# Optimization experiments

Hardware: AMD Instinct MI355X
Metric: run time of the kernel (lower is better)

## Reference

```python
import jax, jax.numpy as jnp
import numpy as np

N, E, IN_FEATS, HID, HEADS = 50000, 800000, 256, 32, 8
NEG_SLOPE = 0.2


def _init_params(key):
    ks = jax.random.split(key, 12)
    def lin(k, fi, fo):
        return jax.random.normal(k, (fi, fo), jnp.float32) * (1.0 / np.sqrt(fi))
    p = {}
    # layer 0: in_feats -> HID x HEADS
    p['W0'] = lin(ks[0], IN_FEATS, HEADS * HID)
    p['al0'] = jax.random.normal(ks[1], (HEADS, HID), jnp.float32) * 0.1
    p['ar0'] = jax.random.normal(ks[2], (HEADS, HID), jnp.float32) * 0.1
    p['b0'] = jnp.zeros((HEADS * HID,), jnp.float32)
    # layer 1: HID*HEADS -> HID x HEADS
    p['W1'] = lin(ks[3], HEADS * HID, HEADS * HID)
    p['al1'] = jax.random.normal(ks[4], (HEADS, HID), jnp.float32) * 0.1
    p['ar1'] = jax.random.normal(ks[5], (HEADS, HID), jnp.float32) * 0.1
    p['b1'] = jnp.zeros((HEADS * HID,), jnp.float32)
    # layer 2 (final): HID*HEADS -> HID x 1 head, no activation
    p['W2'] = lin(ks[6], HEADS * HID, HID)
    p['al2'] = jax.random.normal(ks[7], (1, HID), jnp.float32) * 0.1
    p['ar2'] = jax.random.normal(ks[8], (1, HID), jnp.float32) * 0.1
    p['b2'] = jnp.zeros((HID,), jnp.float32)
    return p


def setup_inputs() -> dict:
    key = jax.random.key(0)
    k1, k2, k3, kp = jax.random.split(key, 4)
    inp = {
        'features': jax.random.normal(k1, (N, IN_FEATS), jnp.float32),
        'src': jax.random.randint(k2, (E,), 0, N, jnp.int32),
        'dst': jax.random.randint(k3, (E,), 0, N, jnp.int32),
    }
    inp.update(_init_params(kp))
    return inp


def _gat_layer(x, src, dst, W, al, ar, b, heads, act):
    n = x.shape[0]
    d = W.shape[1] // heads
    feat = (x @ W).reshape(n, heads, d)           # [N,H,D]
    el = jnp.sum(feat * al, axis=-1)              # [N,H]
    er = jnp.sum(feat * ar, axis=-1)              # [N,H]
    e = jax.nn.leaky_relu(el[src] + er[dst], NEG_SLOPE)   # [E,H]
    # segment softmax over destination neighborhoods
    emax = jax.ops.segment_max(e, dst, num_segments=n)
    ex = jnp.exp(e - emax[dst])
    denom = jax.ops.segment_sum(ex, dst, num_segments=n)
    a = ex / (denom[dst] + 1e-9)                  # [E,H]
    msg = feat[src] * a[:, :, None]               # [E,H,D]
    out = jax.ops.segment_sum(msg, dst, num_segments=n)   # [N,H,D]
    out = out + b.reshape(1, heads, d)
    return act(out) if act is not None else out


def reference(features, src, dst, W0, al0, ar0, b0, W1, al1, ar1, b1, W2, al2, ar2, b2):
    h = _gat_layer(features, src, dst, W0, al0, ar0, b0, HEADS, jax.nn.elu)
    h = h.reshape(h.shape[0], -1)
    h = _gat_layer(h, src, dst, W1, al1, ar1, b1, HEADS, jax.nn.elu)
    h = h.reshape(h.shape[0], -1)
    h = _gat_layer(h, src, dst, W2, al2, ar2, b2, 1, None)   # [N,1,D]
    return h.mean(axis=1)                                    # [N,D]
```

## Files before the change

### kernel.cpp

```cpp
#include <hip/hip_runtime.h>

typedef unsigned short u16;
typedef unsigned int   u32;
typedef __attribute__((ext_vector_type(8))) short  short8;
typedef __attribute__((ext_vector_type(4))) float  f32x4;
typedef __attribute__((ext_vector_type(2))) float  f32x2;
typedef __attribute__((ext_vector_type(2))) unsigned int u32v2;
typedef __attribute__((ext_vector_type(4))) unsigned int u32v4;

#define NN 50000
#define NE 800000

__device__ __forceinline__ float bf2f(u16 b) { return __uint_as_float(((u32)b) << 16); }
__device__ __forceinline__ float bflo(u32 p) { return __uint_as_float(p << 16); }
__device__ __forceinline__ float bfhi(u32 p) { return __uint_as_float(p & 0xffff0000u); }
__device__ __forceinline__ u16 f2bf(float f) {
    u32 u = __float_as_uint(f);
    u32 r = u + 0x7fffu + ((u >> 16) & 1u);
    return (u16)(r >> 16);
}
__device__ __forceinline__ float lexp(float v) {
    v = v > 0.f ? v : 0.2f * v;
    return __expf(fminf(v, 60.f));
}

struct DetectArgs { const u32* p[13]; int nw[13]; };

__global__ __launch_bounds__(256) void k_detect(DetectArgs a, int* flags) {
    __shared__ int sh[256], sz[256];
    int j = blockIdx.x;
    const u32* x = a.p[j];
    int n = a.nw[j];
    int t = threadIdx.x;
    int hits = 0, nz = 0;
    for (int i = t; i < n; i += 256) {
        u32 w = x[i];
        if (w) {
            ++nz;
            u32 e = (w >> 7) & 0xffu;
            if (e >= 100 && e <= 150) ++hits;
        }
    }
    sh[t] = hits; sz[t] = nz;
    __syncthreads();
    for (int ofs = 128; ofs > 0; ofs >>= 1) {
        if (t < ofs) { sh[t] += sh[t + ofs]; sz[t] += sz[t + ofs]; }
        __syncthreads();
    }
    if (t == 0) flags[j] = (sz[0] == 0) ? 2 : ((sh[0] * 2 >= sz[0]) ? 0 : 1);
}

struct ConvArgs { const void* s[9]; float* d[9]; int n[9]; int fi[9]; };

__global__ void k_convert(ConvArgs a, const int* __restrict__ flags) {
    int j = blockIdx.y;
    int i = blockIdx.x * 256 + threadIdx.x;
    if (i >= a.n[j]) return;
    int fl = flags[a.fi[j]];
    float v = 0.f;
    if (fl == 1) v = ((const float*)a.s[j])[i];
    else if (fl == 0) v = bf2f(((const u16*)a.s[j])[i]);
    a.d[j][i] = v;
}

__global__ void k_wpack(const void* __restrict__ Wsrc, const int* __restrict__ flags,
                        int fidx, int N, u16* __restrict__ Wp, int nchunks) {
    int id = blockIdx.x * 256 + threadIdx.x;
    if (id >= nchunks) return;
    int L = id & 63, kt = (id >> 6) & 7, nt = id >> 9;
    int col = nt * 16 + (L & 15);
    int krow = kt * 32 + ((L >> 4) & 3) * 8;
    bool isf32 = (flags[fidx] == 1);
#pragma unroll
    for (int j = 0; j < 8; ++j) {
        int s = (krow + j) * N + col;
        Wp[id * 8 + j] = isf32 ? f2bf(((const float*)Wsrc)[s]) : ((const u16*)Wsrc)[s];
    }
}

__global__ void k_hist(const int* __restrict__ dst, int* __restrict__ deg, int E) {
    int e = blockIdx.x * 256 + threadIdx.x;
    if (e < E) atomicAdd(&deg[dst[e]], 1);
}

__global__ __launch_bounds__(256) void k_scan_partial(const int* __restrict__ deg,
                                                      int* __restrict__ bsum, int n) {
    __shared__ int red[256];
    int t = threadIdx.x;
    int i = blockIdx.x * 256 + t;
    red[t] = (i < n) ? deg[i] : 0;
    __syncthreads();
    for (int ofs = 128; ofs > 0; ofs >>= 1) {
        if (t < ofs) red[t] += red[t + ofs];
        __syncthreads();
    }
    if (t == 0) bsum[blockIdx.x] = red[0];
}

__global__ __launch_bounds__(256) void k_scan_bsum(int* __restrict__ bsum, int nb) {
    __shared__ int s[256];
    int t = threadIdx.x;
    int v = (t < nb) ? bsum[t] : 0;
    s[t] = v;
    __syncthreads();
    for (int ofs = 1; ofs < 256; ofs <<= 1) {
        int x = (t >= ofs) ? s[t - ofs] : 0;
        __syncthreads();
        s[t] += x;
        __syncthreads();
    }
    if (t < nb) bsum[t] = s[t] - v;
}

__global__ __launch_bounds__(256) void k_scan_final(const int* __restrict__ deg,
                                                    const int* __restrict__ bsum,
                                                    int* __restrict__ rowptr,
                                                    int* __restrict__ cursor, int n) {
    __shared__ int s[256];
    int t = threadIdx.x;
    int i = blockIdx.x * 256 + t;
    int v = (i < n) ? deg[i] : 0;
    s[t] = v;
    __syncthreads();
    for (int ofs = 1; ofs < 256; ofs <<= 1) {
        int x = (t >= ofs) ? s[t - ofs] : 0;
        __syncthreads();
        s[t] += x;
        __syncthreads();
    }
    int excl = bsum[blockIdx.x] + s[t] - v;
    if (i < n) {
        rowptr[i] = excl;
        cursor[i] = excl;
        if (i == n - 1) rowptr[n] = excl + v;
    }
}

__global__ void k_scatter(const int* __restrict__ src, const int* __restrict__ dst,
                          int* __restrict__ cursor, int* __restrict__ csr_src, int E) {
    int e = blockIdx.x * 256 + threadIdx.x;
    if (e >= E) return;
    int p = atomicAdd(&cursor[dst[e]], 1);
    csr_src[p] = src[e];
}

__global__ __launch_bounds__(256) void k_gemm_mfma(const void* __restrict__ Xv,
                                                   const int* __restrict__ xflag,
                                                   const u16* __restrict__ Wp,
                                                   u16* __restrict__ OUT, int nrows) {
    __shared__ u16 As[64 * 256];
    const int t = threadIdx.x;
    const int w = t >> 6, L = t & 63;
    const int quad = (L >> 4) & 3;
    const int r0 = blockIdx.x * 64;
    const int nb = blockIdx.y * 8;
    const bool xf32 = (xflag != nullptr) && (*xflag == 1);

    short8* Asv = (short8*)As;
    short8 zero = {0, 0, 0, 0, 0, 0, 0, 0};
#pragma unroll
    for (int i = 0; i < 8; ++i) {
        int g = i * 256 + t;
        int row = g >> 5, cc = g & 31;
        int r = r0 + row;
        short8 val = zero;
        if (r < nrows) {
            if (xf32) {
                const f32x4* Xf4 = (const f32x4*)Xv;
                f32x4 lo = Xf4[(size_t)r * 64 + cc * 2];
                f32x4 hi = Xf4[(size_t)r * 64 + cc * 2 + 1];
                val[0] = (short)f2bf(lo[0]); val[1] = (short)f2bf(lo[1]);
                val[2] = (short)f2bf(lo[2]); val[3] = (short)f2bf(lo[3]);
                val[4] = (short)f2bf(hi[0]); val[5] = (short)f2bf(hi[1]);
                val[6] = (short)f2bf(hi[2]); val[7] = (short)f2bf(hi[3]);
            } else {
                val = ((const short8*)Xv)[(size_t)r * 32 + cc];
            }
        }
        Asv[cc * 64 + row] = val;
    }

    const short8* Wv = (const short8*)Wp;
    short8 bf[2][8];
#pragma unroll
    for (int jn = 0; jn < 2; ++jn) {
        int nt = nb + w + jn * 4;
#pragma unroll
        for (int kt = 0; kt < 8; ++kt) bf[jn][kt] = Wv[(nt * 8 + kt) * 64 + L];
    }
    __syncthreads();

    f32x4 acc[4][2];
#pragma unroll
    for (int mi = 0; mi < 4; ++mi)
#pragma unroll
        for (int jn = 0; jn < 2; ++jn) acc[mi][jn] = (f32x4){0.f, 0.f, 0.f, 0.f};

#pragma unroll
    for (int kt = 0; kt < 8; ++kt) {
#pragma unroll
        for (int mi = 0; mi < 4; ++mi) {
            short8 af = Asv[(kt * 4 + quad) * 64 + mi * 16 + (L & 15)];
            acc[mi][0] = __builtin_amdgcn_mfma_f32_16x16x32_bf16(af, bf[0][kt], acc[mi][0], 0, 0, 0);
            acc[mi][1] = __builtin_amdgcn_mfma_f32_16x16x32_bf16(af, bf[1][kt], acc[mi][1], 0, 0, 0);
        }
    }

    const int colbase = blockIdx.y * 128;
#pragma unroll
    for (int mi = 0; mi < 4; ++mi) {
        int rb = r0 + mi * 16 + quad * 4;
#pragma unroll
        for (int jn = 0; jn < 2; ++jn) {
            int c = colbase + (w + jn * 4) * 16 + (L & 15);
#pragma unroll
            for (int reg = 0; reg < 4; ++reg) {
                int r = rb + reg;
                if (r < nrows) OUT[(size_t)r * 256 + c] = f2bf(acc[mi][jn][reg]);
            }
        }
    }
}

__global__ __launch_bounds__(256) void k_gemm_mfma32(const u16* __restrict__ Xb,
                                                     const u16* __restrict__ Wp,
                                                     u16* __restrict__ OUT, int nrows) {
    __shared__ u16 As[128 * 256];
    const int t = threadIdx.x;
    const int w = t >> 6, L = t & 63;
    const int quad = (L >> 4) & 3;
    const int r0 = blockIdx.x * 128;
    const int mh = (w >> 1) * 64, nt = w & 1;

    const short8* Xv = (const short8*)Xb;
    short8* Asv = (short8*)As;
    short8 zero = {0, 0, 0, 0, 0, 0, 0, 0};
#pragma unroll
    for (int i = 0; i < 16; ++i) {
        int g = i * 256 + t;
        int row = g >> 5, cc = g & 31;
        int r = r0 + row;
        Asv[cc * 128 + row] = (r < nrows) ? Xv[(size_t)r * 32 + cc] : zero;
    }

    const short8* Wv = (const short8*)Wp;
    short8 bf[8];
#pragma unroll
    for (int kt = 0; kt < 8; ++kt) bf[kt] = Wv[(nt * 8 + kt) * 64 + L];
    __syncthreads();

    f32x4 acc[4];
#pragma unroll
    for (int mi = 0; mi < 4; ++mi) acc[mi] = (f32x4){0.f, 0.f, 0.f, 0.f};

#pragma unroll
    for (int kt = 0; kt < 8; ++kt) {
#pragma unroll
        for (int mi = 0; mi < 4; ++mi) {
            short8 af = Asv[(kt * 4 + quad) * 128 + mh + mi * 16 + (L & 15)];
            acc[mi] = __builtin_amdgcn_mfma_f32_16x16x32_bf16(af, bf[kt], acc[mi], 0, 0, 0);
        }
    }

#pragma unroll
    for (int mi = 0; mi < 4; ++mi) {
        int rb = r0 + mh + mi * 16 + quad * 4;
        int c = nt * 16 + (L & 15);
#pragma unroll
        for (int reg = 0; reg < 4; ++reg) {
            int r = rb + reg;
            if (r < nrows) OUT[(size_t)r * 32 + c] = f2bf(acc[mi][reg]);
        }
    }
}

__global__ void k_elr8(const u16* __restrict__ featb, const float* __restrict__ al,
                       const float* __restrict__ ar, float* __restrict__ el,
                       float* __restrict__ er, int n) {
    int idx = blockIdx.x * 256 + threadIdx.x;
    if (idx >= n * 8) return;
    int node = idx >> 3, h = idx & 7;
    const u32v4* fu = (const u32v4*)((const u32*)featb + (size_t)node * 128 + h * 16);
    const float* A = al + h * 32;
    const float* B = ar + h * 32;
    float sl = 0.f, sr = 0.f;
#pragma unroll
    for (int j = 0; j < 4; ++j) {
        u32v4 w4 = fu[j];
#pragma unroll
        for (int k = 0; k < 4; ++k) {
            u32 w = (k == 0) ? w4.x : (k == 1) ? w4.y : (k == 2) ? w4.z : w4.w;
            float f0 = bflo(w), f1 = bfhi(w);
            int c = j * 8 + k * 2;
            sl += f0 * A[c] + f1 * A[c + 1];
            sr += f0 * B[c] + f1 * B[c + 1];
        }
    }
    el[idx] = sl;
    er[idx] = sr;
}

__global__ void k_elr1(const u16* __restrict__ featb, const float* __restrict__ al,
                       const float* __restrict__ ar, float* __restrict__ el,
                       float* __restrict__ er, int n) {
    int node = blockIdx.x * 256 + threadIdx.x;
    if (node >= n) return;
    const u32v4* fu = (const u32v4*)((const u32*)featb + (size_t)node * 16);
    float sl = 0.f, sr = 0.f;
#pragma unroll
    for (int j = 0; j < 4; ++j) {
        u32v4 w4 = fu[j];
#pragma unroll
        for (int k = 0; k < 4; ++k) {
            u32 w = (k == 0) ? w4.x : (k == 1) ? w4.y : (k == 2) ? w4.z : w4.w;
            float f0 = bflo(w), f1 = bfhi(w);
            int c = j * 8 + k * 2;
            sl += f0 * al[c] + f1 * al[c + 1];
            sr += f0 * ar[c] + f1 * ar[c + 1];
        }
    }
    el[node] = sl;
    er[node] = sr;
}

__global__ __launch_bounds__(256) void k_gather8(const int* __restrict__ rowptr,
                                                 const int* __restrict__ csr_src,
                                                 const float* __restrict__ el,
                                                 const float* __restrict__ er,
                                                 const u32v2* __restrict__ featb4,
                                                 const float* __restrict__ bias,
                                                 u32v2* __restrict__ xout4) {
    int t = threadIdx.x;
    int d = blockIdx.x * 4 + (t >> 6);
    int q = t & 63;
    int h = q >> 3;
    int b = rowptr[d], e = rowptr[d + 1];
    float erd = er[d * 8 + h];
    float a0 = 0.f, a1 = 0.f, a2 = 0.f, a3 = 0.f, ssum = 0.f;
    int p = b;
    for (; p + 4 <= e; p += 4) {
        int s0 = csr_src[p], s1 = csr_src[p + 1], s2 = csr_src[p + 2], s3 = csr_src[p + 3];
        float e0 = lexp(el[s0 * 8 + h] + erd);
        float e1 = lexp(el[s1 * 8 + h] + erd);
        float e2 = lexp(el[s2 * 8 + h] + erd);
        float e3 = lexp(el[s3 * 8 + h] + erd);
        u32v2 w0 = featb4[(size_t)s0 * 64 + q];
        u32v2 w1 = featb4[(size_t)s1 * 64 + q];
        u32v2 w2 = featb4[(size_t)s2 * 64 + q];
        u32v2 w3 = featb4[(size_t)s3 * 64 + q];
        a0 += bflo(w0.x) * e0; a1 += bfhi(w0.x) * e0; a2 += bflo(w0.y) * e0; a3 += bfhi(w0.y) * e0;
        a0 += bflo(w1.x) * e1; a1 += bfhi(w1.x) * e1; a2 += bflo(w1.y) * e1; a3 += bfhi(w1.y) * e1;
        a0 += bflo(w2.x) * e2; a1 += bfhi(w2.x) * e2; a2 += bflo(w2.y) * e2; a3 += bfhi(w2.y) * e2;
        a0 += bflo(w3.x) * e3; a1 += bfhi(w3.x) * e3; a2 += bflo(w3.y) * e3; a3 += bfhi(w3.y) * e3;
        ssum += (e0 + e1) + (e2 + e3);
    }
    for (; p < e; ++p) {
        int s = csr_src[p];
        float ev = lexp(el[s * 8 + h] + erd);
        u32v2 w = featb4[(size_t)s * 64 + q];
        a0 += bflo(w.x) * ev; a1 += bfhi(w.x) * ev;
        a2 += bflo(w.y) * ev; a3 += bfhi(w.y) * ev;
        ssum += ev;
    }
    float rd = 1.f / (ssum + 1e-9f);
    const float4 bb = *(const float4*)&bias[4 * q];
    float v0 = a0 * rd + bb.x;
    float v1 = a1 * rd + bb.y;
    float v2 = a2 * rd + bb.z;
    float v3 = a3 * rd + bb.w;
    v0 = v0 > 0.f ? v0 : expm1f(v0);
    v1 = v1 > 0.f ? v1 : expm1f(v1);
    v2 = v2 > 0.f ? v2 : expm1f(v2);
    v3 = v3 > 0.f ? v3 : expm1f(v3);
    u32v2 o;
    o.x = (u32)f2bf(v0) | ((u32)f2bf(v1) << 16);
    o.y = (u32)f2bf(v2) | ((u32)f2bf(v3) << 16);
    xout4[(size_t)d * 64 + q] = o;
}

__global__ __launch_bounds__(256) void k_gather1(const int* __restrict__ rowptr,
                                                 const int* __restrict__ csr_src,
                                                 const float* __restrict__ el,
                                                 const float* __restrict__ er,
                                                 const u32* __restrict__ featb2,
                                                 const float* __restrict__ bias,
                                                 void* __restrict__ out,
                                                 const int* __restrict__ flag, int n) {
    int t = threadIdx.x;
    int d = blockIdx.x * 16 + (t >> 4);
    int q = t & 15;
    if (d >= n) return;
    int b = rowptr[d], e = rowptr[d + 1];
    float erd = er[d];
    float a0 = 0.f, a1 = 0.f, ssum = 0.f;
    int p = b;
    for (; p + 4 <= e; p += 4) {
        int s0 = csr_src[p], s1 = csr_src[p + 1], s2 = csr_src[p + 2], s3 = csr_src[p + 3];
        float e0 = lexp(el[s0] + erd);
        float e1 = lexp(el[s1] + erd);
        float e2 = lexp(el[s2] + erd);
        float e3 = lexp(el[s3] + erd);
        u32 w0 = featb2[(size_t)s0 * 16 + q];
        u32 w1 = featb2[(size_t)s1 * 16 + q];
        u32 w2 = featb2[(size_t)s2 * 16 + q];
        u32 w3 = featb2[(size_t)s3 * 16 + q];
        a0 += bflo(w0) * e0; a1 += bfhi(w0) * e0;
        a0 += bflo(w1) * e1; a1 += bfhi(w1) * e1;
        a0 += bflo(w2) * e2; a1 += bfhi(w2) * e2;
        a0 += bflo(w3) * e3; a1 += bfhi(w3) * e3;
        ssum += (e0 + e1) + (e2 + e3);
    }
    for (; p < e; ++p) {
        int s = csr_src[p];
        float ev = lexp(el[s] + erd);
        u32 w = featb2[(size_t)s * 16 + q];
        a0 += bflo(w) * ev;
        a1 += bfhi(w) * ev;
        ssum += ev;
    }
    float rd = 1.f / (ssum + 1e-9f);
    float v0 = a0 * rd + bias[2 * q];
    float v1 = a1 * rd + bias[2 * q + 1];
    if (*flag == 1) {
        f32x2 o = {v0, v1};
        ((f32x2*)out)[(size_t)d * 16 + q] = o;
    } else {
        ((u32*)out)[(size_t)d * 16 + q] = (u32)f2bf(v0) | ((u32)f2bf(v1) << 16);
    }
}

extern "C" void kernel_launch(void* const* d_in, const int* in_sizes, int n_in,
                              void* d_out, int out_size, void* d_ws, size_t ws_size,
                              hipStream_t stream) {
    const void* features = d_in[0];
    const int* src = (const int*)d_in[1];
    const int* dst = (const int*)d_in[2];

    char* ws = (char*)d_ws;
    size_t off = 0;
    auto carve = [&](size_t bytes) -> void* {
        void* p = ws + off;
        off = (off + bytes + 255) & ~(size_t)255;
        return p;
    };
    int*   flags = (int*)carve(64);
    float* pconv = (float*)carve(2048 * 4);
    u16*   Wp0 = (u16*)carve(65536 * 2);
    u16*   Wp1 = (u16*)carve(65536 * 2);
    u16*   Wp2 = (u16*)carve(8192 * 2);
    u16*   Xb    = (u16*)carve((size_t)NN * 256 * 2);
    u16*   featb = (u16*)carve((size_t)NN * 256 * 2);
    float* el   = (float*)carve((size_t)NN * 8 * 4);
    float* er   = (float*)carve((size_t)NN * 8 * 4);
    int*   deg     = (int*)carve((size_t)NN * 4);
    int*   cursor  = (int*)carve((size_t)NN * 4);
    int*   rowptr  = (int*)carve((size_t)(NN + 1) * 4);
    int*   bsum    = (int*)carve(256 * 4);
    int*   csr_src = (int*)carve((size_t)NE * 4);
    if (off > ws_size) return;

    const int N = NN, E = NE;
    const int nscan = (N + 255) / 256;

    DetectArgs da;
    const int din_idx[13] = {0, 3, 4, 5, 6, 7, 8, 9, 10, 11, 12, 13, 14};
    for (int j = 0; j < 13; ++j) {
        da.p[j] = (const u32*)d_in[din_idx[j]];
        int nw = in_sizes[din_idx[j]] / 2;
        da.nw[j] = nw > 512 ? 512 : nw;
    }
    k_detect<<<13, 256, 0, stream>>>(da, flags);

    ConvArgs ca;
    const int psl[9] = {4, 5, 6, 8, 9, 10, 12, 13, 14};
    const int pfl[9] = {2, 3, 4, 6, 7, 8, 10, 11, 12};
    float* dsts[9];
    {
        size_t o = 0;
        for (int j = 0; j < 9; ++j) {
            dsts[j] = pconv + o;
            o += (size_t)in_sizes[psl[j]];
        }
    }
    for (int j = 0; j < 9; ++j) {
        ca.s[j] = d_in[psl[j]];
        ca.d[j] = dsts[j];
        ca.n[j] = in_sizes[psl[j]];
        ca.fi[j] = pfl[j];
    }
    k_convert<<<dim3(1, 9), 256, 0, stream>>>(ca, flags);
    float* al0f = dsts[0]; float* ar0f = dsts[1]; float* b0f = dsts[2];
    float* al1f = dsts[3]; float* ar1f = dsts[4]; float* b1f = dsts[5];
    float* al2f = dsts[6]; float* ar2f = dsts[7]; float* b2f = dsts[8];

    k_wpack<<<32, 256, 0, stream>>>(d_in[3],  flags, 1, 256, Wp0, 8192);
    k_wpack<<<32, 256, 0, stream>>>(d_in[7],  flags, 5, 256, Wp1, 8192);
    k_wpack<<<4,  256, 0, stream>>>(d_in[11], flags, 9, 32,  Wp2, 1024);

    hipMemsetAsync(deg, 0, (size_t)N * 4, stream);
    k_hist<<<(E + 255) / 256, 256, 0, stream>>>(dst, deg, E);
    k_scan_partial<<<nscan, 256, 0, stream>>>(deg, bsum, N);
    k_scan_bsum<<<1, 256, 0, stream>>>(bsum, nscan);
    k_scan_final<<<nscan, 256, 0, stream>>>(deg, bsum, rowptr, cursor, N);
    k_scatter<<<(E + 255) / 256, 256, 0, stream>>>(src, dst, cursor, csr_src, E);

    const dim3 ggrid((N + 63) / 64, 2);

    k_gemm_mfma<<<ggrid, 256, 0, stream>>>(features, flags, Wp0, featb, N);
    k_elr8<<<(N * 8 + 255) / 256, 256, 0, stream>>>(featb, al0f, ar0f, el, er, N);
    k_gather8<<<N / 4, 256, 0, stream>>>(rowptr, csr_src, el, er,
                                         (const u32v2*)featb, b0f, (u32v2*)Xb);

    k_gemm_mfma<<<ggrid, 256, 0, stream>>>(Xb, nullptr, Wp1, featb, N);
    k_elr8<<<(N * 8 + 255) / 256, 256, 0, stream>>>(featb, al1f, ar1f, el, er, N);
    k_gather8<<<N / 4, 256, 0, stream>>>(rowptr, csr_src, el, er,
                                         (const u32v2*)featb, b1f, (u32v2*)Xb);

    k_gemm_mfma32<<<(N + 127) / 128, 256, 0, stream>>>(Xb, Wp2, featb, N);
    k_elr1<<<(N + 255) / 256, 256, 0, stream>>>(featb, al2f, ar2f, el, er, N);
    k_gather1<<<(N + 15) / 16, 256, 0, stream>>>(rowptr, csr_src, el, er,
                                                 (const u32*)featb, b2f,
                                                 d_out, flags, N);
}
```

Baseline: 444.7 us.

## Swizzle GEMM LDS layout and restructure gather8 to per-head blocks with shuffled edges

Adds an XOR swizzle on the LDS row index in both MFMA GEMM kernels to reduce bank conflicts on the transposed A-tile reads. Rewrites the 8-head gather so each block handles one head for 16 destination nodes. Within each 16-lane group, lanes cooperatively load edge sources and attention weights, then broadcast them via shuffles. Each lane accumulates 2 features from a 64-byte per-head slice. This trades wide per-node rows for more blocks, computing each edge's exp once per head instead of in 8 redundant lanes. It also rewrites leaky ReLU as fmax.

```diff
diff --git a/kernel.cpp b/kernel.cpp
--- a/kernel.cpp
+++ b/kernel.cpp
@@ -20,7 +20,7 @@
     return (u16)(r >> 16);
 }
 __device__ __forceinline__ float lexp(float v) {
-    v = v > 0.f ? v : 0.2f * v;
+    v = fmaxf(v, 0.2f * v);
     return __expf(fminf(v, 60.f));
 }
 
@@ -177,7 +177,7 @@
                 val = ((const short8*)Xv)[(size_t)r * 32 + cc];
             }
         }
-        Asv[cc * 64 + row] = val;
+        Asv[cc * 64 + (row ^ (cc & 7))] = val;
     }
 
     const short8* Wv = (const short8*)Wp;
@@ -198,9 +198,10 @@
 
 #pragma unroll
     for (int kt = 0; kt < 8; ++kt) {
+        const int ccr = kt * 4 + quad;
 #pragma unroll
         for (int mi = 0; mi < 4; ++mi) {
-            short8 af = Asv[(kt * 4 + quad) * 64 + mi * 16 + (L & 15)];
+            short8 af = Asv[ccr * 64 + ((mi * 16 + (L & 15)) ^ (ccr & 7))];
             acc[mi][0] = __builtin_amdgcn_mfma_f32_16x16x32_bf16(af, bf[0][kt], acc[mi][0], 0, 0, 0);
             acc[mi][1] = __builtin_amdgcn_mfma_f32_16x16x32_bf16(af, bf[1][kt], acc[mi][1], 0, 0, 0);
         }
@@ -240,7 +241,7 @@
         int g = i * 256 + t;
         int row = g >> 5, cc = g & 31;
         int r = r0 + row;
-        Asv[cc * 128 + row] = (r < nrows) ? Xv[(size_t)r * 32 + cc] : zero;
+        Asv[cc * 128 + (row ^ (cc & 7))] = (r < nrows) ? Xv[(size_t)r * 32 + cc] : zero;
     }
 
     const short8* Wv = (const short8*)Wp;
@@ -255,9 +256,10 @@
 
 #pragma unroll
     for (int kt = 0; kt < 8; ++kt) {
+        const int ccr = kt * 4 + quad;
 #pragma unroll
         for (int mi = 0; mi < 4; ++mi) {
-            short8 af = Asv[(kt * 4 + quad) * 128 + mh + mi * 16 + (L & 15)];
+            short8 af = Asv[ccr * 128 + ((mh + mi * 16 + (L & 15)) ^ (ccr & 7))];
             acc[mi] = __builtin_amdgcn_mfma_f32_16x16x32_bf16(af, bf[kt], acc[mi], 0, 0, 0);
         }
     }
@@ -327,55 +329,46 @@
                                                  const int* __restrict__ csr_src,
                                                  const float* __restrict__ el,
                                                  const float* __restrict__ er,
-                                                 const u32v2* __restrict__ featb4,
+                                                 const u32* __restrict__ featb2,
                                                  const float* __restrict__ bias,
-                                                 u32v2* __restrict__ xout4) {
-    int t = threadIdx.x;
-    int d = blockIdx.x * 4 + (t >> 6);
-    int q = t & 63;
-    int h = q >> 3;
-    int b = rowptr[d], e = rowptr[d + 1];
-    float erd = er[d * 8 + h];
-    float a0 = 0.f, a1 = 0.f, a2 = 0.f, a3 = 0.f, ssum = 0.f;
-    int p = b;
-    for (; p + 4 <= e; p += 4) {
-        int s0 = csr_src[p], s1 = csr_src[p + 1], s2 = csr_src[p + 2], s3 = csr_src[p + 3];
-        float e0 = lexp(el[s0 * 8 + h] + erd);
-        float e1 = lexp(el[s1 * 8 + h] + erd);
-        float e2 = lexp(el[s2 * 8 + h] + erd);
-        float e3 = lexp(el[s3 * 8 + h] + erd);
-        u32v2 w0 = featb4[(size_t)s0 * 64 + q];
-        u32v2 w1 = featb4[(size_t)s1 * 64 + q];
-        u32v2 w2 = featb4[(size_t)s2 * 64 + q];
-        u32v2 w3 = featb4[(size_t)s3 * 64 + q];
-        a0 += bflo(w0.x) * e0; a1 += bfhi(w0.x) * e0; a2 += bflo(w0.y) * e0; a3 += bfhi(w0.y) * e0;
-        a0 += bflo(w1.x) * e1; a1 += bfhi(w1.x) * e1; a2 += bflo(w1.y) * e1; a3 += bfhi(w1.y) * e1;
-        a0 += bflo(w2.x) * e2; a1 += bfhi(w2.x) * e2; a2 += bflo(w2.y) * e2; a3 += bfhi(w2.y) * e2;
-        a0 += bflo(w3.x) * e3; a1 += bfhi(w3.x) * e3; a2 += bflo(w3.y) * e3; a3 += bfhi(w3.y) * e3;
-        ssum += (e0 + e1) + (e2 + e3);
-    }
-    for (; p < e; ++p) {
-        int s = csr_src[p];
-        float ev = lexp(el[s * 8 + h] + erd);
-        u32v2 w = featb4[(size_t)s * 64 + q];
-        a0 += bflo(w.x) * ev; a1 += bfhi(w.x) * ev;
-        a2 += bflo(w.y) * ev; a3 += bfhi(w.y) * ev;
-        ssum += ev;
-    }
-    float rd = 1.f / (ssum + 1e-9f);
-    const float4 bb = *(const float4*)&bias[4 * q];
-    float v0 = a0 * rd + bb.x;
-    float v1 = a1 * rd + bb.y;
-    float v2 = a2 * rd + bb.z;
-    float v3 = a3 * rd + bb.w;
+                                                 u32* __restrict__ xout2) {
+    const int t = threadIdx.x;
+    const int h = blockIdx.x & 7;
+    const int g = blockIdx.x >> 3;
+    const int d = g * 16 + (t >> 4);
+    const int lane = t & 15;
+    const int b = rowptr[d], e = rowptr[d + 1];
+    const float erd = er[d * 8 + h];
+    const u32* __restrict__ fp = featb2 + h * 16 + lane;
+    float a0 = 0.f, a1 = 0.f, ssum = 0.f;
+
+    for (int c = b; c < e; c += 16) {
+        const int idx = c + lane;
+        const int s_own = csr_src[idx < e ? idx : e - 1];
+        const float ex_own = (idx < e) ? lexp(el[s_own * 8 + h] + erd) : 0.f;
+        ssum += ex_own;
+#pragma unroll
+        for (int i = 0; i < 16; ++i) {
+            const int si = __shfl(s_own, i, 16);
+            const float ai = __shfl(ex_own, i, 16);
+            const u32 w = fp[(size_t)si * 128];
+            a0 += bflo(w) * ai;
+            a1 += bfhi(w) * ai;
+        }
+    }
+
+    ssum += __shfl_xor(ssum, 1);
+    ssum += __shfl_xor(ssum, 2);
+    ssum += __shfl_xor(ssum, 4);
+    ssum += __shfl_xor(ssum, 8);
+
+    const float rd = 1.f / (ssum + 1e-9f);
+    const f32x2 bb = *(const f32x2*)&bias[h * 32 + lane * 2];
+    float v0 = a0 * rd + bb[0];
+    float v1 = a1 * rd + bb[1];
     v0 = v0 > 0.f ? v0 : expm1f(v0);
     v1 = v1 > 0.f ? v1 : expm1f(v1);
-    v2 = v2 > 0.f ? v2 : expm1f(v2);
-    v3 = v3 > 0.f ? v3 : expm1f(v3);
-    u32v2 o;
-    o.x = (u32)f2bf(v0) | ((u32)f2bf(v1) << 16);
-    o.y = (u32)f2bf(v2) | ((u32)f2bf(v3) << 16);
-    xout4[(size_t)d * 64 + q] = o;
+    xout2[(size_t)d * 128 + h * 16 + lane] = (u32)f2bf(v0) | ((u32)f2bf(v1) << 16);
 }
 
 __global__ __launch_bounds__(256) void k_gather1(const int* __restrict__ rowptr,
@@ -505,16 +498,17 @@
     k_scatter<<<(E + 255) / 256, 256, 0, stream>>>(src, dst, cursor, csr_src, E);
 
     const dim3 ggrid((N + 63) / 64, 2);
+    const int ggrid8 = 8 * (N / 16);
 
     k_gemm_mfma<<<ggrid, 256, 0, stream>>>(features, flags, Wp0, featb, N);
     k_elr8<<<(N * 8 + 255) / 256, 256, 0, stream>>>(featb, al0f, ar0f, el, er, N);
-    k_gather8<<<N / 4, 256, 0, stream>>>(rowptr, csr_src, el, er,
-                                         (const u32v2*)featb, b0f, (u32v2*)Xb);
+    k_gather8<<<ggrid8, 256, 0, stream>>>(rowptr, csr_src, el, er,
+                                          (const u32*)featb, b0f, (u32*)Xb);
 
     k_gemm_mfma<<<ggrid, 256, 0, stream>>>(Xb, nullptr, Wp1, featb, N);
     k_elr8<<<(N * 8 + 255) / 256, 256, 0, stream>>>(featb, al1f, ar1f, el, er, N);
-    k_gather8<<<N / 4, 256, 0, stream>>>(rowptr, csr_src, el, er,
-                                         (const u32v2*)featb, b1f, (u32v2*)Xb);
+    k_gather8<<<ggrid8, 256, 0, stream>>>(rowptr, csr_src, el, er,
+                                          (const u32*)featb, b1f, (u32*)Xb);
 
     k_gemm_mfma32<<<(N + 127) / 128, 256, 0, stream>>>(Xb, Wp2, featb, N);
     k_elr1<<<(N + 255) / 256, 256, 0, stream>>>(featb, al2f, ar2f, el, er, N);
```

Result: slower. 531.9 us (+19.6%).
